# Optimization experiments

Measured on AMD Instinct MI355X. Metric: run time of the kernel, lower is better.

The kernel has to match this reference:

```python
import jax, jax.numpy as jnp
import numpy as np

ENC_DIM = 1024
EMB_DIM = 256
K = 8192          # codebook size
COMMIT = 0.25
LN_EPS = 1e-5


def _ln(x, g, b):
    m = jnp.mean(x, axis=-1, keepdims=True)
    v = jnp.mean(jnp.square(x - m), axis=-1, keepdims=True)
    return (x - m) * jax.lax.rsqrt(v + LN_EPS) * g + b


def _mlp(x, W1, b1, g1, be1, W2, b2, g2, be2):
    # two feed_forward blocks: Linear -> ReLU -> LayerNorm
    x = _ln(jax.nn.relu(x @ W1 + b1), g1, be1)
    x = _ln(jax.nn.relu(x @ W2 + b2), g2, be2)
    return x


def setup_inputs() -> dict:
    key = jax.random.key(0)
    ks = jax.random.split(key, 10)
    d = ENC_DIM
    s = 1.0 / np.sqrt(d)
    inp = {"x": jax.random.normal(ks[0], (4, 2048, d), dtype=jnp.float32)}
    # encoder MLP (2 blocks)
    inp["We1"] = jax.random.uniform(ks[1], (d, d), jnp.float32, -s, s)
    inp["be1"] = jnp.zeros((d,), jnp.float32)
    inp["ge1"] = jnp.ones((d,), jnp.float32)
    inp["bne1"] = jnp.zeros((d,), jnp.float32)
    inp["We2"] = jax.random.uniform(ks[2], (d, d), jnp.float32, -s, s)
    inp["be2"] = jnp.zeros((d,), jnp.float32)
    inp["ge2"] = jnp.ones((d,), jnp.float32)
    inp["bne2"] = jnp.zeros((d,), jnp.float32)
    # decoder MLP (2 blocks)
    inp["Wd1"] = jax.random.uniform(ks[3], (d, d), jnp.float32, -s, s)
    inp["bd1"] = jnp.zeros((d,), jnp.float32)
    inp["gd1"] = jnp.ones((d,), jnp.float32)
    inp["bnd1"] = jnp.zeros((d,), jnp.float32)
    inp["Wd2"] = jax.random.uniform(ks[4], (d, d), jnp.float32, -s, s)
    inp["bd2"] = jnp.zeros((d,), jnp.float32)
    inp["gd2"] = jnp.ones((d,), jnp.float32)
    inp["bnd2"] = jnp.zeros((d,), jnp.float32)
    # codebook, init uniform(-1/K, 1/K)
    inp["codebook"] = jax.random.uniform(ks[5], (K, EMB_DIM), jnp.float32, -1.0 / K, 1.0 / K)
    return inp


def reference(x, We1, be1, ge1, bne1, We2, be2, ge2, bne2,
              Wd1, bd1, gd1, bnd1, Wd2, bd2, gd2, bnd2, codebook):
    bs, seq_len, d = x.shape
    z = _mlp(x, We1, be1, ge1, bne1, We2, be2, ge2, bne2)

    # ---- VectorQuantizer ----
    zg = z.reshape(bs, seq_len, -1, EMB_DIM)              # (b, s, g, e)
    flat = zg.reshape(-1, EMB_DIM)                        # (N, e)
    # pairwise squared distances to codebook: (N, K)
    dist = (jnp.sum(flat * flat, axis=1, keepdims=True)
            + jnp.sum(codebook * codebook, axis=1)
            - 2.0 * flat @ codebook.T)
    idx = jnp.argmin(dist, axis=1)                        # (N,)
    quantized = jnp.take(codebook, idx, axis=0).reshape(zg.shape)

    e_latent = jnp.mean(jnp.square(jax.lax.stop_gradient(quantized) - zg))
    q_latent = jnp.mean(jnp.square(quantized - jax.lax.stop_gradient(zg)))
    loss = q_latent + COMMIT * e_latent

    # straight-through estimator
    quantized = zg + jax.lax.stop_gradient(quantized - zg)
    quantized = quantized.reshape(bs, seq_len, d)

    # perplexity from code usage histogram
    n = flat.shape[0]
    counts = jnp.zeros((K,), x.dtype).at[idx].add(1.0)
    avg_probs = counts / n
    perplexity = jnp.exp(-jnp.sum(avg_probs * jnp.log(avg_probs + 1e-10)))

    out = _mlp(quantized, Wd1, bd1, gd1, bnd1, Wd2, bd2, gd2, bnd2)
    return (out, loss, perplexity)
```

## Files before the change

kernel.cpp:

```cpp
#include <hip/hip_runtime.h>
#include <stdint.h>


typedef short bf16x8 __attribute__((ext_vector_type(8)));
typedef float f32x4 __attribute__((ext_vector_type(4)));

__device__ __forceinline__ void gl2lds16(const void* g, void* l) {
  __builtin_amdgcn_global_load_lds(
      (const __attribute__((address_space(1))) void*)g,
      (__attribute__((address_space(3))) void*)l, 16, 0, 0);
}

__device__ __forceinline__ float bf2f(unsigned short u) {
  return __uint_as_float(((unsigned)u) << 16);
}
__device__ __forceinline__ unsigned short f2bf(float f) {
  unsigned x = __float_as_uint(f);
  unsigned r = (x + 0x7fffu + ((x >> 16) & 1u)) >> 16;
  return (unsigned short)r;
}
__device__ __forceinline__ unsigned long long packScore(float s, int code) {
  unsigned u = __float_as_uint(s);
  u = (u & 0x80000000u) ? ~u : (u | 0x80000000u);
  return ((unsigned long long)u << 32) | (unsigned)code;
}
__device__ __forceinline__ unsigned long long shflxor_u64(unsigned long long v, int m) {
  union { unsigned long long u; int i[2]; } a;
  a.u = v;
  a.i[0] = __shfl_xor(a.i[0], m);
  a.i[1] = __shfl_xor(a.i[1], m);
  return a.u;
}

__global__ __launch_bounds__(256)
void cast_bf16(const float* __restrict__ X, unsigned short* __restrict__ Y, int n4) {
  int i = blockIdx.x * 256 + threadIdx.x;
  if (i < n4) {
    float4 v = ((const float4*)X)[i];
    ushort4 o = make_ushort4(f2bf(v.x), f2bf(v.y), f2bf(v.z), f2bf(v.w));
    ((ushort4*)Y)[i] = o;
  }
}

__global__ __launch_bounds__(256)
void transpose_cast(const float* __restrict__ W, unsigned short* __restrict__ Wt, int D) {
  __shared__ float s[32][33];
  int tx = threadIdx.x & 31, ty = threadIdx.x >> 5;
  int bx = blockIdx.x, by = blockIdx.y;
#pragma unroll
  for (int p = 0; p < 4; p++) {
    int r = by * 32 + ty + p * 8, c = bx * 32 + tx;
    s[ty + p * 8][tx] = W[(size_t)r * D + c];
  }
  __syncthreads();
#pragma unroll
  for (int p = 0; p < 4; p++) {
    int r = bx * 32 + ty + p * 8, c = by * 32 + tx;
    Wt[(size_t)r * D + c] = f2bf(s[tx][ty + p * 8]);
  }
}

__global__ __launch_bounds__(256)
void code_norms(const float* __restrict__ cb, float* __restrict__ cn) {
  int row = blockIdx.x * 4 + (threadIdx.x >> 6);
  int lane = threadIdx.x & 63;
  float4 v = ((const float4*)(cb + (size_t)row * 256))[lane];
  float s = v.x * v.x + v.y * v.y + v.z * v.z + v.w * v.w;
#pragma unroll
  for (int off = 32; off > 0; off >>= 1) s += __shfl_down(s, off);
  if (lane == 0) cn[row] = s;
}

__global__ __launch_bounds__(256, 2)
void gemm_bias_relu(const unsigned short* __restrict__ A, const unsigned short* __restrict__ Bt,
                    const float* __restrict__ bias, unsigned short* __restrict__ C,
                    int M, int N, int K) {
  __shared__ unsigned short As[128 * 64];
  __shared__ unsigned short Bs[128 * 64];
  const int t = threadIdx.x;
  const int wv = t >> 6, lane = t & 63;
  const int wm = wv >> 1, wn = wv & 1;
  const int quad = lane >> 4, l15 = lane & 15;
  const int row0 = blockIdx.y * 128, col0 = blockIdx.x * 128;
  const int rsub = lane >> 3;
  const int dchunk = (lane & 7) ^ rsub;

  f32x4 acc[4][4];
#pragma unroll
  for (int i = 0; i < 4; i++)
#pragma unroll
    for (int j = 0; j < 4; j++) acc[i][j] = (f32x4){0.f, 0.f, 0.f, 0.f};

  for (int k0 = 0; k0 < K; k0 += 64) {
#pragma unroll
    for (int j = 0; j < 4; j++) {
      int slab = j * 4 + wv;
      int row = slab * 8 + rsub;
      gl2lds16(A + (size_t)(row0 + row) * K + k0 + dchunk * 8, As + slab * 512);
      gl2lds16(Bt + (size_t)(col0 + row) * K + k0 + dchunk * 8, Bs + slab * 512);
    }
    __syncthreads();
#pragma unroll
    for (int kk = 0; kk < 2; kk++) {
      bf16x8 af[4], bfr[4];
#pragma unroll
      for (int mt = 0; mt < 4; mt++) {
        int row = wm * 64 + mt * 16 + l15;
        af[mt] = *(const bf16x8*)(As + row * 64 + (((kk * 4 + quad) ^ (l15 & 7)) * 8));
      }
#pragma unroll
      for (int nt = 0; nt < 4; nt++) {
        int row = wn * 64 + nt * 16 + l15;
        bfr[nt] = *(const bf16x8*)(Bs + row * 64 + (((kk * 4 + quad) ^ (l15 & 7)) * 8));
      }
#pragma unroll
      for (int mt = 0; mt < 4; mt++)
#pragma unroll
        for (int nt = 0; nt < 4; nt++)
          acc[mt][nt] = __builtin_amdgcn_mfma_f32_16x16x32_bf16(af[mt], bfr[nt], acc[mt][nt], 0, 0, 0);
    }
    __syncthreads();
  }
#pragma unroll
  for (int mt = 0; mt < 4; mt++) {
#pragma unroll
    for (int nt = 0; nt < 4; nt++) {
      int col = col0 + wn * 64 + nt * 16 + l15;
      float b = bias[col];
#pragma unroll
      for (int r = 0; r < 4; r++) {
        int row = row0 + wm * 64 + mt * 16 + quad * 4 + r;
        float v = acc[mt][nt][r] + b;
        C[(size_t)row * N + col] = f2bf(v > 0.f ? v : 0.f);
      }
    }
  }
}

__global__ __launch_bounds__(256)
void ln_kernel(const unsigned short* __restrict__ X, const float* __restrict__ g,
               const float* __restrict__ b, unsigned short* __restrict__ obf,
               float* __restrict__ of32) {
  const int row = blockIdx.x, t = threadIdx.x;
  ushort4 u = ((const ushort4*)(X + (size_t)row * 1024))[t];
  float4 v = make_float4(bf2f(u.x), bf2f(u.y), bf2f(u.z), bf2f(u.w));
  float s = v.x + v.y + v.z + v.w;
  float ss = v.x * v.x + v.y * v.y + v.z * v.z + v.w * v.w;
#pragma unroll
  for (int off = 32; off > 0; off >>= 1) {
    s += __shfl_down(s, off);
    ss += __shfl_down(ss, off);
  }
  __shared__ float rs[4], rss[4];
  const int wave = t >> 6, lane = t & 63;
  if (lane == 0) { rs[wave] = s; rss[wave] = ss; }
  __syncthreads();
  float S = rs[0] + rs[1] + rs[2] + rs[3];
  float SS = rss[0] + rss[1] + rss[2] + rss[3];
  float m = S * (1.0f / 1024.0f);
  float var = SS * (1.0f / 1024.0f) - m * m;
  float rstd = 1.0f / sqrtf(var + 1e-5f);
  float4 gv = ((const float4*)g)[t];
  float4 bv = ((const float4*)b)[t];
  float4 o;
  o.x = (v.x - m) * rstd * gv.x + bv.x;
  o.y = (v.y - m) * rstd * gv.y + bv.y;
  o.z = (v.z - m) * rstd * gv.z + bv.z;
  o.w = (v.w - m) * rstd * gv.w + bv.w;
  if (obf) {
    ushort4 q = make_ushort4(f2bf(o.x), f2bf(o.y), f2bf(o.z), f2bf(o.w));
    ((ushort4*)(obf + (size_t)row * 1024))[t] = q;
  } else {
    ((float4*)(of32 + (size_t)row * 1024))[t] = o;
  }
}

__global__ __launch_bounds__(256, 2)
void vq_dist(const unsigned short* __restrict__ Z, const unsigned short* __restrict__ Cb,
             const float* __restrict__ cnorm, unsigned long long* __restrict__ bestg) {
  __shared__ unsigned short Bs[2][64 * 256];
  __shared__ unsigned long long runmin[64];
  const int t = threadIdx.x;
  const int wv = t >> 6, lane = t & 63;
  const int quad = lane >> 4, l15 = lane & 15;
  const int row0 = blockIdx.x * 64;

  if (t < 64) runmin[t] = ~0ull;

  bf16x8 zf[4][8];
#pragma unroll
  for (int mt = 0; mt < 4; mt++)
#pragma unroll
    for (int ks = 0; ks < 8; ks++)
      zf[mt][ks] = *(const bf16x8*)(Z + (size_t)(row0 + mt * 16 + l15) * 256 + ks * 32 + quad * 8);

  float msc[4][4];
  int mcd[4][4];
#pragma unroll
  for (int mt = 0; mt < 4; mt++)
#pragma unroll
    for (int r = 0; r < 4; r++) { msc[mt][r] = 3.4e38f; mcd[mt][r] = 0; }

  const int dcode = lane >> 5;
  const int dgr = lane & 31;

  const unsigned short* gbase = Cb + (size_t)(64 + wv * 16 + l15) * 256 + quad * 8;
  const int slot = wv * 16 + l15;
  const int rxor = l15 & 7;

#pragma unroll
  for (int j = 0; j < 8; j++) {
    int slab = wv * 8 + j;
    int sl = slab * 2 + dcode;
    gl2lds16(Cb + (size_t)sl * 256 + ((dgr ^ (sl & 7)) * 8), &Bs[0][slab * 512]);
  }
  bf16x8 gbuf[2];
  gbuf[0] = *(const bf16x8*)(gbase);

  for (int ch = 0; ch < 64; ch++) {
    __builtin_amdgcn_s_waitcnt(0x3F70);

    const int cur = ch & 1;
    if (ch + 1 < 64) {
      const int cb2 = (ch + 1) * 128;
#pragma unroll
      for (int j = 0; j < 8; j++) {
        int slab = wv * 8 + j;
        int sl = slab * 2 + dcode;
        gl2lds16(Cb + (size_t)(cb2 + sl) * 256 + ((dgr ^ (sl & 7)) * 8),
                 &Bs[cur ^ 1][slab * 512]);
      }
    }
    float cn0 = cnorm[ch * 128 + slot];
    float cn1 = cnorm[ch * 128 + 64 + slot];

    bf16x8 lbuf[2];
    lbuf[0] = *(const bf16x8*)(&Bs[cur][slot * 256 + ((quad ^ rxor) * 8)]);

    f32x4 acc[4][2];
#pragma unroll
    for (int ks = 0; ks < 8; ks++) {
      if (ks < 7)
        lbuf[(ks + 1) & 1] =
            *(const bf16x8*)(&Bs[cur][slot * 256 + ((((ks + 1) * 4 + quad) ^ rxor) * 8)]);
      {
        const size_t noff = (ks == 7) ? (size_t)((ch + 1) & 63) * 32768
                                      : (size_t)ch * 32768 + (size_t)(ks + 1) * 32;
        gbuf[(ks + 1) & 1] = *(const bf16x8*)(gbase + noff);
      }
      bf16x8 lb = lbuf[ks & 1], gb = gbuf[ks & 1];
      if (ks == 0) {
        const f32x4 z4 = (f32x4){0.f, 0.f, 0.f, 0.f};
#pragma unroll
        for (int mt = 0; mt < 4; mt++) {
          acc[mt][0] = __builtin_amdgcn_mfma_f32_16x16x32_bf16(zf[mt][0], lb, z4, 0, 0, 0);
          acc[mt][1] = __builtin_amdgcn_mfma_f32_16x16x32_bf16(zf[mt][0], gb, z4, 0, 0, 0);
        }
      } else {
#pragma unroll
        for (int mt = 0; mt < 4; mt++) {
          acc[mt][0] = __builtin_amdgcn_mfma_f32_16x16x32_bf16(zf[mt][ks], lb, acc[mt][0], 0, 0, 0);
          acc[mt][1] = __builtin_amdgcn_mfma_f32_16x16x32_bf16(zf[mt][ks], gb, acc[mt][1], 0, 0, 0);
        }
      }
    }
#pragma unroll
    for (int p = 0; p < 2; p++) {
      int code = ch * 128 + p * 64 + slot;
      float cn = p == 0 ? cn0 : cn1;
#pragma unroll
      for (int mt = 0; mt < 4; mt++)
#pragma unroll
        for (int r = 0; r < 4; r++) {
          float sc = cn - 2.0f * acc[mt][p][r];
          if (sc < msc[mt][r]) { msc[mt][r] = sc; mcd[mt][r] = code; }
        }
    }
  }

  __syncthreads();
#pragma unroll
  for (int mt = 0; mt < 4; mt++) {
#pragma unroll
    for (int r = 0; r < 4; r++) {
      unsigned long long bp = packScore(msc[mt][r], mcd[mt][r]);
#pragma unroll
      for (int m = 1; m < 16; m <<= 1) {
        unsigned long long o = shflxor_u64(bp, m);
        bp = o < bp ? o : bp;
      }
      if (l15 == 0) atomicMin(&runmin[mt * 16 + quad * 4 + r], bp);
    }
  }
  __syncthreads();
  if (t < 64) bestg[row0 + t] = runmin[t];
}

__global__ __launch_bounds__(256)
void vq_gather(const unsigned long long* __restrict__ bestg, const float* __restrict__ cb,
               const unsigned short* __restrict__ zb, unsigned short* __restrict__ qb,
               int* __restrict__ counts, float* __restrict__ lpart) {
  const int wave = threadIdx.x >> 6;
  const int g = blockIdx.x * 4 + wave;
  const int lane = threadIdx.x & 63;
  const int idx = (int)(bestg[g] & 0xFFFFFFFFull);
  float4 c = ((const float4*)(cb + (size_t)idx * 256))[lane];
  ushort4 q = make_ushort4(f2bf(c.x), f2bf(c.y), f2bf(c.z), f2bf(c.w));
  ((ushort4*)(qb + (size_t)g * 256))[lane] = q;
  ushort4 z = ((const ushort4*)(zb + (size_t)g * 256))[lane];
  float dx = c.x - bf2f(z.x), dy = c.y - bf2f(z.y);
  float dz = c.z - bf2f(z.z), dw = c.w - bf2f(z.w);
  float p = dx * dx + dy * dy + dz * dz + dw * dw;
#pragma unroll
  for (int off = 32; off > 0; off >>= 1) p += __shfl_down(p, off);
  __shared__ float sp[4];
  if (lane == 0) {
    sp[wave] = p;
    atomicAdd(&counts[idx], 1);
  }
  __syncthreads();
  if (threadIdx.x == 0) lpart[blockIdx.x] = sp[0] + sp[1] + sp[2] + sp[3];
}

__global__ __launch_bounds__(256)
void finalize(const int* __restrict__ counts, const float* __restrict__ lpart,
              float* __restrict__ out2) {
  const int t = threadIdx.x;
  double h = 0.0, l = 0.0;
  for (int i = t; i < 8192; i += 256) {
    double pr = (double)counts[i] * (1.0 / 32768.0);
    h += pr * log(pr + 1e-10);
    l += (double)lpart[i];
  }
  __shared__ double sh[256], sl[256];
  sh[t] = h;
  sl[t] = l;
  __syncthreads();
  for (int w = 128; w > 0; w >>= 1) {
    if (t < w) { sh[t] += sh[t + w]; sl[t] += sl[t + w]; }
    __syncthreads();
  }
  if (t == 0) {
    out2[0] = (float)(1.25 * sl[0] * (1.0 / 8388608.0));
    out2[1] = (float)exp(-sh[0]);
  }
}

extern "C" void kernel_launch(void* const* d_in, const int* in_sizes, int n_in,
                              void* d_out, int out_size, void* d_ws, size_t ws_size,
                              hipStream_t stream) {
  const float* x = (const float*)d_in[0];
  const float* We1 = (const float*)d_in[1];
  const float* be1 = (const float*)d_in[2];
  const float* ge1 = (const float*)d_in[3];
  const float* bne1 = (const float*)d_in[4];
  const float* We2 = (const float*)d_in[5];
  const float* be2 = (const float*)d_in[6];
  const float* ge2 = (const float*)d_in[7];
  const float* bne2 = (const float*)d_in[8];
  const float* Wd1 = (const float*)d_in[9];
  const float* bd1 = (const float*)d_in[10];
  const float* gd1 = (const float*)d_in[11];
  const float* bnd1 = (const float*)d_in[12];
  const float* Wd2 = (const float*)d_in[13];
  const float* bd2 = (const float*)d_in[14];
  const float* gd2 = (const float*)d_in[15];
  const float* bnd2 = (const float*)d_in[16];
  const float* codebook = (const float*)d_in[17];
  float* out = (float*)d_out;

  char* w = (char*)d_ws;
  auto alloc = [&](size_t bytes) -> char* {
    char* p = w;
    w += (bytes + 255) & ~(size_t)255;
    return p;
  };
  unsigned short* xb = (unsigned short*)alloc((size_t)8192 * 1024 * 2);
  unsigned short* wt0 = (unsigned short*)alloc((size_t)1024 * 1024 * 2);
  unsigned short* wt1 = (unsigned short*)alloc((size_t)1024 * 1024 * 2);
  unsigned short* wt2 = (unsigned short*)alloc((size_t)1024 * 1024 * 2);
  unsigned short* wt3 = (unsigned short*)alloc((size_t)1024 * 1024 * 2);
  unsigned short* cbb = (unsigned short*)alloc((size_t)8192 * 256 * 2);
  float* cnorm = (float*)alloc((size_t)8192 * 4);
  unsigned short* act = (unsigned short*)alloc((size_t)8192 * 1024 * 2);
  unsigned short* yb = (unsigned short*)alloc((size_t)8192 * 1024 * 2);
  unsigned short* zb = (unsigned short*)alloc((size_t)8192 * 1024 * 2);
  unsigned short* qb = (unsigned short*)alloc((size_t)8192 * 1024 * 2);
  unsigned long long* best = (unsigned long long*)alloc((size_t)32768 * 8);
  int* counts = (int*)alloc((size_t)8192 * 4);
  float* lpart = (float*)alloc((size_t)8192 * 4);

  hipMemsetAsync(counts, 0, (size_t)8192 * 4, stream);

  cast_bf16<<<(2097152 + 255) / 256, 256, 0, stream>>>(x, xb, 2097152);
  dim3 tg(32, 32);
  transpose_cast<<<tg, 256, 0, stream>>>(We1, wt0, 1024);
  transpose_cast<<<tg, 256, 0, stream>>>(We2, wt1, 1024);
  transpose_cast<<<tg, 256, 0, stream>>>(Wd1, wt2, 1024);
  transpose_cast<<<tg, 256, 0, stream>>>(Wd2, wt3, 1024);
  cast_bf16<<<(524288 + 255) / 256, 256, 0, stream>>>(codebook, cbb, 524288);
  code_norms<<<2048, 256, 0, stream>>>(codebook, cnorm);

  dim3 gg(8, 64);
  gemm_bias_relu<<<gg, 256, 0, stream>>>(xb, wt0, be1, act, 8192, 1024, 1024);
  ln_kernel<<<8192, 256, 0, stream>>>(act, ge1, bne1, yb, nullptr);
  gemm_bias_relu<<<gg, 256, 0, stream>>>(yb, wt1, be2, act, 8192, 1024, 1024);
  ln_kernel<<<8192, 256, 0, stream>>>(act, ge2, bne2, zb, nullptr);
  vq_dist<<<512, 256, 0, stream>>>(zb, cbb, cnorm, best);
  vq_gather<<<8192, 256, 0, stream>>>(best, codebook, zb, qb, counts, lpart);
  gemm_bias_relu<<<gg, 256, 0, stream>>>(qb, wt2, bd1, act, 8192, 1024, 1024);
  ln_kernel<<<8192, 256, 0, stream>>>(act, gd1, bnd1, yb, nullptr);
  gemm_bias_relu<<<gg, 256, 0, stream>>>(yb, wt3, bd2, act, 8192, 1024, 1024);
  ln_kernel<<<8192, 256, 0, stream>>>(act, gd2, bnd2, nullptr, out);

  finalize<<<1, 256, 0, stream>>>(counts, lpart, out + 8388608);
}
```

Before: 484.8 us.

## Stream all codebook chunks through LDS and defer the argmin by one chunk

```diff
diff --git a/kernel.cpp b/kernel.cpp
--- a/kernel.cpp
+++ b/kernel.cpp
@@ -203,8 +203,6 @@
 
   const int dcode = lane >> 5;
   const int dgr = lane & 31;
-
-  const unsigned short* gbase = Cb + (size_t)(64 + wv * 16 + l15) * 256 + quad * 8;
   const int slot = wv * 16 + l15;
   const int rxor = l15 & 7;
 
@@ -214,15 +212,18 @@
     int sl = slab * 2 + dcode;
     gl2lds16(Cb + (size_t)sl * 256 + ((dgr ^ (sl & 7)) * 8), &Bs[0][slab * 512]);
   }
-  bf16x8 gbuf[2];
-  gbuf[0] = *(const bf16x8*)(gbase);
-
-  for (int ch = 0; ch < 64; ch++) {
+  float cn_cur = cnorm[slot];
+  float cn_prev = 3.4e38f;
+  f32x4 pacc[4];
+#pragma unroll
+  for (int mt = 0; mt < 4; mt++) pacc[mt] = (f32x4){0.f, 0.f, 0.f, 0.f};
+
+  for (int ch = 0; ch < 128; ch++) {
+    const int cur = ch & 1;
     __builtin_amdgcn_s_waitcnt(0x3F70);
 
-    const int cur = ch & 1;
-    if (ch + 1 < 64) {
-      const int cb2 = (ch + 1) * 128;
+    {
+      const int cb2 = ((ch + 1) & 127) * 64;
 #pragma unroll
       for (int j = 0; j < 8; j++) {
         int slab = wv * 8 + j;
@@ -231,51 +232,52 @@
                  &Bs[cur ^ 1][slab * 512]);
       }
     }
-    float cn0 = cnorm[ch * 128 + slot];
-    float cn1 = cnorm[ch * 128 + 64 + slot];
-
-    bf16x8 lbuf[2];
+    float cn_next = cnorm[(((ch + 1) & 127) * 64) + slot];
+
+    bf16x8 lbuf[3];
     lbuf[0] = *(const bf16x8*)(&Bs[cur][slot * 256 + ((quad ^ rxor) * 8)]);
-
-    f32x4 acc[4][2];
+    lbuf[1] = *(const bf16x8*)(&Bs[cur][slot * 256 + (((4 + quad) ^ rxor) * 8)]);
+
+    {
+      int code = (ch - 1) * 64 + slot;
+#pragma unroll
+      for (int mt = 0; mt < 4; mt++)
+#pragma unroll
+        for (int r = 0; r < 4; r++) {
+          float sc = cn_prev - 2.0f * pacc[mt][r];
+          if (sc < msc[mt][r]) { msc[mt][r] = sc; mcd[mt][r] = code; }
+        }
+    }
+
 #pragma unroll
     for (int ks = 0; ks < 8; ks++) {
-      if (ks < 7)
-        lbuf[(ks + 1) & 1] =
-            *(const bf16x8*)(&Bs[cur][slot * 256 + ((((ks + 1) * 4 + quad) ^ rxor) * 8)]);
-      {
-        const size_t noff = (ks == 7) ? (size_t)((ch + 1) & 63) * 32768
-                                      : (size_t)ch * 32768 + (size_t)(ks + 1) * 32;
-        gbuf[(ks + 1) & 1] = *(const bf16x8*)(gbase + noff);
-      }
-      bf16x8 lb = lbuf[ks & 1], gb = gbuf[ks & 1];
+      if (ks + 2 < 8)
+        lbuf[(ks + 2) % 3] =
+            *(const bf16x8*)(&Bs[cur][slot * 256 + ((((ks + 2) * 4 + quad) ^ rxor) * 8)]);
+      bf16x8 lb = lbuf[ks % 3];
       if (ks == 0) {
         const f32x4 z4 = (f32x4){0.f, 0.f, 0.f, 0.f};
 #pragma unroll
-        for (int mt = 0; mt < 4; mt++) {
-          acc[mt][0] = __builtin_amdgcn_mfma_f32_16x16x32_bf16(zf[mt][0], lb, z4, 0, 0, 0);
-          acc[mt][1] = __builtin_amdgcn_mfma_f32_16x16x32_bf16(zf[mt][0], gb, z4, 0, 0, 0);
-        }
+        for (int mt = 0; mt < 4; mt++)
+          pacc[mt] = __builtin_amdgcn_mfma_f32_16x16x32_bf16(zf[mt][0], lb, z4, 0, 0, 0);
       } else {
 #pragma unroll
-        for (int mt = 0; mt < 4; mt++) {
-          acc[mt][0] = __builtin_amdgcn_mfma_f32_16x16x32_bf16(zf[mt][ks], lb, acc[mt][0], 0, 0, 0);
-          acc[mt][1] = __builtin_amdgcn_mfma_f32_16x16x32_bf16(zf[mt][ks], gb, acc[mt][1], 0, 0, 0);
-        }
-      }
-    }
-#pragma unroll
-    for (int p = 0; p < 2; p++) {
-      int code = ch * 128 + p * 64 + slot;
-      float cn = p == 0 ? cn0 : cn1;
-#pragma unroll
-      for (int mt = 0; mt < 4; mt++)
-#pragma unroll
-        for (int r = 0; r < 4; r++) {
-          float sc = cn - 2.0f * acc[mt][p][r];
-          if (sc < msc[mt][r]) { msc[mt][r] = sc; mcd[mt][r] = code; }
-        }
-    }
+        for (int mt = 0; mt < 4; mt++)
+          pacc[mt] = __builtin_amdgcn_mfma_f32_16x16x32_bf16(zf[mt][ks], lb, pacc[mt], 0, 0, 0);
+      }
+    }
+    cn_prev = cn_cur;
+    cn_cur = cn_next;
+  }
+  {
+    int code = 127 * 64 + slot;
+#pragma unroll
+    for (int mt = 0; mt < 4; mt++)
+#pragma unroll
+      for (int r = 0; r < 4; r++) {
+        float sc = cn_prev - 2.0f * pacc[mt][r];
+        if (sc < msc[mt][r]) { msc[mt][r] = sc; mcd[mt][r] = code; }
+      }
   }
 
   __syncthreads();
```

Result: faster. 465.1 us (-4.1%).
